# Kernel tuning notes

Hardware: AMD Instinct MI355X
Metric: run time of the kernel (lower is better)

The kernel has to match this reference:

```python
import jax, jax.numpy as jnp
import numpy as np

EPS_STD = 1e-6
EPS_LN = 1e-5


def layernorm(x, g, b):
    m = jnp.mean(x, axis=-1, keepdims=True)
    v = jnp.mean((x - m) ** 2, axis=-1, keepdims=True)
    return (x - m) * jax.lax.rsqrt(v + EPS_LN) * g + b


def res_block(x, w1, b1, g1, bb1, w2, b2, g2, bb2):
    # in_dim == out_dim for all blocks here -> skip is Identity
    h = jax.nn.relu(layernorm(x @ w1 + b1, g1, bb1))
    h = layernorm(h @ w2 + b2, g2, bb2)
    return jax.nn.relu(h + x)


def setup_inputs() -> dict:
    key = jax.random.key(0)
    ks = jax.random.split(key, 12)
    B, N, C_in, C_out, K, M = 8, 2048, 64, 128, 24, 1024
    D = 2 * C_in  # 128 == C_out
    inp = {
        'features': jax.random.normal(ks[0], (B, N, C_in), jnp.float32),
        'xyz': jax.random.normal(ks[1], (B, N, 3), jnp.float32),
        'fps_idx': jax.random.randint(ks[2], (B, M), 0, N, jnp.int32),
        'alpha': jnp.ones((1, 1, 1, C_in), jnp.float32),
        'beta': jnp.zeros((1, 1, 1, C_in), jnp.float32),
    }
    # stacked params for 2 pre blocks (D->D) and 2 pos blocks (C_out->C_out); D == C_out
    def blk(k, n, d):
        k1, k2 = jax.random.split(k)
        return dict(
            w1=jax.random.normal(k1, (n, d, d), jnp.float32) * 0.05,
            b1=jnp.zeros((n, 1, d), jnp.float32),
            g1=jnp.ones((n, 1, d), jnp.float32),
            bb1=jnp.zeros((n, 1, d), jnp.float32),
            w2=jax.random.normal(k2, (n, d, d), jnp.float32) * 0.05,
            b2=jnp.zeros((n, 1, d), jnp.float32),
            g2=jnp.ones((n, 1, d), jnp.float32),
            bb2=jnp.zeros((n, 1, d), jnp.float32),
        )
    for pfx, k in (('pre', ks[3]), ('pos', ks[4])):
        for name, v in blk(k, 2, D).items():
            inp[pfx + '_' + name] = v
    return inp


def reference(features, xyz, fps_idx, alpha, beta,
              pre_w1, pre_b1, pre_g1, pre_bb1, pre_w2, pre_b2, pre_g2, pre_bb2,
              pos_w1, pos_b1, pos_g1, pos_bb1, pos_w2, pos_b2, pos_g2, pos_bb2):
    B, N, C = features.shape
    K = 24
    # kNN on xyz via squared distances (same ordering as cdist topk smallest)
    x2 = jnp.sum(xyz * xyz, axis=-1)  # (B,N)
    d2 = x2[:, :, None] + x2[:, None, :] - 2.0 * jnp.einsum('bnd,bmd->bnm', xyz, xyz)
    _, idx = jax.lax.top_k(-d2, K)  # (B,N,K)
    gather = jax.vmap(lambda f, i: f[i])
    grouped = gather(features, idx)  # (B,N,K,C)
    # GeometricAffine: normalize over neighbor dim (torch std is unbiased, ddof=1)
    mean = jnp.mean(grouped, axis=-2, keepdims=True)
    std = jnp.maximum(jnp.std(grouped, axis=-2, keepdims=True, ddof=1), EPS_STD)
    grouped = (grouped - mean) / std * alpha + beta
    center = features[:, :, None, :]
    local = jnp.concatenate(
        [jnp.broadcast_to(center, grouped.shape), grouped - center], axis=-1)  # (B,N,K,2C)
    h = local.reshape(B * N * K, 2 * C)
    for i in range(pre_w1.shape[0]):
        h = res_block(h, pre_w1[i], pre_b1[i], pre_g1[i], pre_bb1[i],
                      pre_w2[i], pre_b2[i], pre_g2[i], pre_bb2[i])
    h = h.reshape(B, N, K, -1).max(axis=2)  # (B,N,C_out)
    h = h.reshape(B * N, -1)
    for i in range(pos_w1.shape[0]):
        h = res_block(h, pos_w1[i], pos_b1[i], pos_g1[i], pos_bb1[i],
                      pos_w2[i], pos_b2[i], pos_g2[i], pos_bb2[i])
    h = h.reshape(B, N, -1)
    new_xyz = gather(xyz, fps_idx)
    new_features = gather(h, fps_idx)
    return new_features, new_xyz
```

## Files before the change

kernel.cpp:

```cpp
#include <hip/hip_runtime.h>


typedef _Float16 half8 __attribute__((ext_vector_type(8)));
typedef _Float16 h2v   __attribute__((ext_vector_type(2)));
typedef float    f32x4 __attribute__((ext_vector_type(4)));
typedef unsigned long long u64;

#define DEVINL __device__ __forceinline__

union H8 { half8 v; h2v p[4]; int w[4]; };

DEVINL f32x4 splat4(float s) { f32x4 r = {s, s, s, s}; return r; }

DEVINL _Float16 hmax1(_Float16 a, _Float16 b) { return a > b ? a : b; }
DEVINL h2v hmax2v(h2v a, h2v b) {
  h2v r; r[0] = hmax1(a[0], b[0]); r[1] = hmax1(a[1], b[1]); return r;
}
DEVINL h2v cvt2h(float lo, float hi) {
  return __builtin_bit_cast(h2v, __builtin_amdgcn_cvt_pkrtz(lo, hi));
}
DEVINL half8 hmax8(half8 a, half8 b) {
  H8 A, B, R; A.v = a; B.v = b;
  #pragma unroll
  for (int e = 0; e < 4; ++e) R.p[e] = hmax2v(A.p[e], B.p[e]);
  return R.v;
}
DEVINL half8 shfl_h8(half8 x, int m) {
  H8 X; X.v = x;
  #pragma unroll
  for (int e = 0; e < 4; ++e) X.w[e] = __shfl_xor(X.w[e], m);
  return X.v;
}

DEVINL float dpp_add16(float x) {
  int v = __builtin_bit_cast(int, x);
  x += __builtin_bit_cast(float, __builtin_amdgcn_update_dpp(v, v, 0xB1, 0xF, 0xF, true));
  v = __builtin_bit_cast(int, x);
  x += __builtin_bit_cast(float, __builtin_amdgcn_update_dpp(v, v, 0x4E, 0xF, 0xF, true));
  v = __builtin_bit_cast(int, x);
  x += __builtin_bit_cast(float, __builtin_amdgcn_update_dpp(v, v, 0x141, 0xF, 0xF, true));
  v = __builtin_bit_cast(int, x);
  x += __builtin_bit_cast(float, __builtin_amdgcn_update_dpp(v, v, 0x140, 0xF, 0xF, true));
  return x;
}

DEVINL void stH(_Float16* L, int row, int col, _Float16 v) {
  const int b2 = col * 2;
  *(_Float16*)((char*)L + row * 256 + (((b2 >> 4) ^ (row & 7)) << 4) + (b2 & 15)) = v;
}
DEVINL half8 ldA(const _Float16* L, int row, int ch) {
  return *(const half8*)((const char*)L + row * 256 + ((ch ^ (row & 7)) << 4));
}
DEVINL void stA(_Float16* L, int row, int ch, half8 v) {
  *(half8*)((char*)L + row * 256 + ((ch ^ (row & 7)) << 4)) = v;
}

template<int MT>
DEVINL void mm_dev(const _Float16* L, const _Float16* __restrict__ W, f32x4 acc[MT][9], int lane) {
  const int g = lane >> 4, r = lane & 15;
  #pragma unroll
  for (int s = 0; s < 4; ++s) {
    half8 bfr[9];
    #pragma unroll
    for (int t = 0; t < 9; ++t)
      bfr[t] = *(const half8*)(W + (((s * 9 + t) * 64 + lane) * 8));
    #pragma unroll
    for (int mt = 0; mt < MT; ++mt) {
      const half8 a = ldA(L, mt * 16 + r, s * 4 + g);
      #pragma unroll
      for (int t = 0; t < 9; ++t)
        acc[mt][t] = __builtin_amdgcn_mfma_f32_16x16x32_f16(a, bfr[t], acc[mt][t], 0, 0, 0);
    }
  }
}

template<int MT>
DEVINL void epi_ln(f32x4 acc[MT][9], const float* __restrict__ bv, const float* __restrict__ gv,
                   const float* __restrict__ bbv, int lane) {
  const int cr = lane & 15;
  const f32x4 bp0 = *(const f32x4*)(bv + cr * 8),  bp1 = *(const f32x4*)(bv + cr * 8 + 4);
  const f32x4 gp0 = *(const f32x4*)(gv + cr * 8),  gp1 = *(const f32x4*)(gv + cr * 8 + 4);
  const f32x4 ap0 = *(const f32x4*)(bbv + cr * 8), ap1 = *(const f32x4*)(bbv + cr * 8 + 4);
  const f32x4 bs4 = bp0 + bp1;
  const float sb = dpp_add16(bs4[0] + bs4[1] + bs4[2] + bs4[3]);
  #pragma unroll
  for (int mt = 0; mt < MT; ++mt) {
    f32x4 sq4 = splat4(0.f);
    #pragma unroll
    for (int t = 0; t < 8; ++t) {
      const float bias = (t < 4) ? bp0[t & 3] : bp1[t & 3];
      acc[mt][t] = acc[mt][t] + splat4(bias);
      sq4 = sq4 + acc[mt][t] * acc[mt][t];
    }
    #pragma unroll
    for (int q = 0; q < 4; ++q) sq4[q] = dpp_add16(sq4[q]);
    const f32x4 mean = (acc[mt][8] + splat4(sb)) * splat4(1.f / 128.f);
    f32x4 rstd;
    #pragma unroll
    for (int q = 0; q < 4; ++q) {
      const float var = fmaxf(sq4[q] * (1.f / 128.f) - mean[q] * mean[q], 0.f);
      rstd[q] = rsqrtf(var + 1e-5f);
    }
    #pragma unroll
    for (int t = 0; t < 8; ++t) {
      const float gs = (t < 4) ? gp0[t & 3] : gp1[t & 3];
      const float as = (t < 4) ? ap0[t & 3] : ap1[t & 3];
      acc[mt][t] = (acc[mt][t] - mean) * rstd * splat4(gs) + splat4(as);
    }
  }
}

template<int MT, int MODE>
DEVINL void res_block_dev(_Float16* L, const _Float16* __restrict__ W1, const _Float16* __restrict__ W2,
                          const float* b1, const float* g1, const float* bb1,
                          const float* b2, const float* g2, const float* bb2,
                          half8 xres[MT][4], int lane, float* __restrict__ gdst) {
  const int g = lane >> 4, cr = lane & 15;
  const h2v zero2 = {(_Float16)0, (_Float16)0};
  f32x4 acc[MT][9];
  #pragma unroll
  for (int mt = 0; mt < MT; ++mt)
    #pragma unroll
    for (int t = 0; t < 9; ++t) acc[mt][t] = splat4(0.f);
  mm_dev<MT>(L, W1, acc, lane);
  epi_ln<MT>(acc, b1, g1, bb1, lane);
  __threadfence_block();
  #pragma unroll
  for (int mt = 0; mt < MT; ++mt)
    #pragma unroll
    for (int q = 0; q < 4; ++q) {
      H8 hv;
      #pragma unroll
      for (int e = 0; e < 4; ++e)
        hv.p[e] = hmax2v(cvt2h(acc[mt][2 * e][q], acc[mt][2 * e + 1][q]), zero2);
      stA(L, mt * 16 + 4 * g + q, cr, hv.v);
    }
  #pragma unroll
  for (int mt = 0; mt < MT; ++mt)
    #pragma unroll
    for (int t = 0; t < 9; ++t) acc[mt][t] = splat4(0.f);
  __threadfence_block();
  mm_dev<MT>(L, W2, acc, lane);
  epi_ln<MT>(acc, b2, g2, bb2, lane);
  if constexpr (MODE == 0) __threadfence_block();
  #pragma unroll
  for (int mt = 0; mt < MT; ++mt)
    #pragma unroll
    for (int q = 0; q < 4; ++q) {
      const int row = mt * 16 + 4 * g + q;
      if constexpr (MODE == 2) {
        f32x4 lo, hi;
        #pragma unroll
        for (int e = 0; e < 4; ++e) {
          lo[e] = fmaxf(acc[mt][e][q]     + (float)xres[mt][q][e],     0.f);
          hi[e] = fmaxf(acc[mt][e + 4][q] + (float)xres[mt][q][e + 4], 0.f);
        }
        *(f32x4*)(gdst + row * 128 + cr * 8)     = lo;
        *(f32x4*)(gdst + row * 128 + cr * 8 + 4) = hi;
      } else {
        H8 s;
        #pragma unroll
        for (int e = 0; e < 4; ++e)
          s.p[e] = cvt2h(acc[mt][2 * e][q], acc[mt][2 * e + 1][q]);
        H8 z; z.v = s.v + xres[mt][q];
        #pragma unroll
        for (int e = 0; e < 4; ++e) z.p[e] = hmax2v(z.p[e], zero2);
        xres[mt][q] = z.v;
        if constexpr (MODE == 0) stA(L, row, cr, z.v);
      }
    }
  if constexpr (MODE == 0) __threadfence_block();
}

__global__ __launch_bounds__(256) void k_pack(const float* __restrict__ preW1, const float* __restrict__ preW2,
                                              const float* __restrict__ posW1, const float* __restrict__ posW2,
                                              _Float16* __restrict__ wp) {
  const int o = blockIdx.x * 256 + threadIdx.x;
  const int mat = o / 18432, rem = o % 18432;
  const int frag = rem >> 9, li = (rem >> 3) & 63, j = rem & 7;
  const int s = frag / 9, t = frag % 9;
  const int k = s * 32 + ((li >> 4) << 3) + j;
  const int blk = (mat >> 1) & 1, which = mat & 1;
  const float* base = (mat < 4) ? (which ? preW2 : preW1) : (which ? posW2 : posW1);
  const float* Wm = base + blk * 16384;
  float val;
  if (t < 8) {
    val = Wm[k * 128 + (li & 15) * 8 + t];
  } else {
    float ssum = 0.f;
    for (int n = 0; n < 128; ++n) ssum += Wm[k * 128 + n];
    val = ssum;
  }
  wp[o] = (_Float16)val;
}

DEVINL u64 kmin(u64 a, u64 b) { return a < b ? a : b; }
DEVINL u64 kmax(u64 a, u64 b) { return a > b ? a : b; }
DEVINL u64 min8(const u64* k) {
  u64 a = kmin(k[0], k[1]), b = kmin(k[2], k[3]);
  u64 c = kmin(k[4], k[5]), d = kmin(k[6], k[7]);
  return kmin(kmin(a, b), kmin(c, d));
}
DEVINL void inv8(u64* k, int j) {
  #pragma unroll
  for (int s = 0; s < 8; ++s) k[s] = (s == j) ? ~0ULL : k[s];
}
DEVINL u64 bitonic64(u64 v, int lane) {
  #pragma unroll
  for (int k = 2; k <= 64; k <<= 1) {
    #pragma unroll
    for (int j = k >> 1; j > 0; j >>= 1) {
      const u64 o = __shfl_xor(v, j);
      const bool up = ((lane & k) == 0);
      const bool lower = ((lane & j) == 0);
      v = (lower == up) ? kmin(v, o) : kmax(v, o);
    }
  }
  return v;
}

__global__ __launch_bounds__(256) void k_knn(const float* __restrict__ xyz, int* __restrict__ idxout) {
  __shared__ float sx[2048], sy[2048], sz[2048];
  __shared__ u64 scand[4][64];
  const int b = blockIdx.x >> 9;
  const int qbase = (blockIdx.x & 511) * 4;
  const float* xb = xyz + (size_t)b * 2048 * 3;
  for (int i = threadIdx.x; i < 2048; i += 256) {
    sx[i] = xb[i * 3 + 0]; sy[i] = xb[i * 3 + 1]; sz[i] = xb[i * 3 + 2];
  }
  __syncthreads();
  const int wid = threadIdx.x >> 6, lane = threadIdx.x & 63;
  const int q = qbase + wid;
  const float qx = sx[q], qy = sy[q], qz = sz[q];
  const float q2 = qx * qx + qy * qy + qz * qz;
  u64 key[32];
  u64 lmin = ~0ULL;
  #pragma unroll
  for (int j = 0; j < 32; ++j) {
    const int m = j * 64 + lane;
    const float mx = sx[m], my = sy[m], mz = sz[m];
    const float m2 = mx * mx + my * my + mz * mz;
    const float d = fmaxf(q2 + m2 - 2.f * (qx * mx + qy * my + qz * mz), 0.f);
    key[j] = ((u64)__builtin_bit_cast(unsigned, d) << 32) | (unsigned)m;
    lmin = kmin(lmin, key[j]);
  }
  const u64 t = __shfl(bitonic64(lmin, lane), 23);
  int c = 0;
  #pragma unroll
  for (int j = 0; j < 32; ++j) c += (key[j] <= t) ? 1 : 0;
  int inc = c;
  #pragma unroll
  for (int off = 1; off < 64; off <<= 1) {
    const int n = __shfl_up(inc, off);
    if (lane >= off) inc += n;
  }
  const int T = __shfl(inc, 63);
  if (T <= 64) {
    int idx = inc - c;
    #pragma unroll
    for (int j = 0; j < 32; ++j)
      if (key[j] <= t) { scand[wid][idx] = key[j]; ++idx; }
    __threadfence_block();
    u64 cand = (lane < T) ? scand[wid][lane] : ~0ULL;
    cand = bitonic64(cand, lane);
    if (lane < 24) idxout[(size_t)(b * 2048 + q) * 24 + lane] = (int)(unsigned)cand;
  } else {
    u64 gk[4];
    #pragma unroll
    for (int g4 = 0; g4 < 4; ++g4) gk[g4] = min8(key + g4 * 8);
    int keep = 0;
    #pragma unroll 1
    for (int r = 0; r < 24; ++r) {
      u64 kk = kmin(kmin(gk[0], gk[1]), kmin(gk[2], gk[3]));
      #pragma unroll
      for (int off = 32; off >= 1; off >>= 1) kk = kmin(__shfl_xor(kk, off), kk);
      const unsigned wm = (unsigned)kk;
      if (lane == r) keep = (int)wm;
      if (lane == (int)(wm & 63)) {
        const int j = (int)(wm >> 6);
        if (j < 16) {
          if (j < 8) { inv8(key,      j);      gk[0] = min8(key);      }
          else       { inv8(key + 8,  j - 8);  gk[1] = min8(key + 8);  }
        } else {
          if (j < 24){ inv8(key + 16, j - 16); gk[2] = min8(key + 16); }
          else       { inv8(key + 24, j - 24); gk[3] = min8(key + 24); }
        }
      }
    }
    if (lane < 24) idxout[(size_t)(b * 2048 + q) * 24 + lane] = keep;
  }
}

__global__ __launch_bounds__(256, 1) void k_pre(
    const float* __restrict__ features, const int* __restrict__ idxin,
    const _Float16* __restrict__ wp, const float* __restrict__ alpha, const float* __restrict__ beta,
    const float* __restrict__ b1, const float* __restrict__ g1, const float* __restrict__ bb1,
    const float* __restrict__ b2, const float* __restrict__ g2, const float* __restrict__ bb2,
    _Float16* __restrict__ h0) {
  __shared__ _Float16 lds[4][48 * 128];
  const int wid = threadIdx.x >> 6, lane = threadIdx.x & 63;
  _Float16* L = lds[wid];
  const int wgl = blockIdx.x * 4 + wid;
  const int p0 = wgl * 2;
  const int b = p0 >> 11;
  const float* fb = features + (size_t)b * 2048 * 64;
  {
    const int c = lane;
    const float al = alpha[c], be = beta[c];
    #pragma unroll 1
    for (int pp = 0; pp < 2; ++pp) {
      const int p = p0 + pp;
      const int n = p & 2047;
      const int* ip = idxin + (size_t)p * 24;
      const float center = fb[n * 64 + c];
      float v[24]; float su = 0.f, sq = 0.f;
      #pragma unroll
      for (int k = 0; k < 24; ++k) {
        v[k] = fb[ip[k] * 64 + c];
        su += v[k]; sq = fmaf(v[k], v[k], sq);
      }
      const float mean = su * (1.f / 24.f);
      const float var = fmaxf((sq - 24.f * mean * mean) * (1.f / 23.f), 0.f);
      const float rs = 1.f / fmaxf(sqrtf(var), 1e-6f);
      const float c1 = rs * al;
      const float c0 = be - mean * c1 - center;
      const _Float16 ch = (_Float16)center;
      #pragma unroll
      for (int k = 0; k < 24; ++k) {
        const int row = pp * 24 + k;
        stH(L, row, c, ch);
        stH(L, row, 64 + c, (_Float16)fmaf(v[k], c1, c0));
      }
    }
  }
  __threadfence_block();
  const int g = lane >> 4, cr = lane & 15;
  half8 xres[3][4];
  #pragma unroll
  for (int mt = 0; mt < 3; ++mt)
    #pragma unroll
    for (int q = 0; q < 4; ++q)
      xres[mt][q] = ldA(L, mt * 16 + 4 * g + q, cr);
  res_block_dev<3, 0>(L, wp,         wp + 18432,  b1,       g1,       bb1,       b2,       g2,       bb2,       xres, lane, nullptr);
  res_block_dev<3, 1>(L, wp + 36864, wp + 55296,  b1 + 128, g1 + 128, bb1 + 128, b2 + 128, g2 + 128, bb2 + 128, xres, lane, nullptr);
  half8 m0 = hmax8(hmax8(xres[0][0], xres[0][1]), hmax8(xres[0][2], xres[0][3]));
  m0 = hmax8(m0, shfl_h8(m0, 16));
  m0 = hmax8(m0, shfl_h8(m0, 32));
  half8 m1 = hmax8(hmax8(xres[1][0], xres[1][1]), hmax8(xres[1][2], xres[1][3]));
  m1 = hmax8(m1, shfl_h8(m1, 16));
  const half8 m1o = shfl_h8(m1, 32);
  half8 m2 = hmax8(hmax8(xres[2][0], xres[2][1]), hmax8(xres[2][2], xres[2][3]));
  m2 = hmax8(m2, shfl_h8(m2, 16));
  m2 = hmax8(m2, shfl_h8(m2, 32));
  if (g == 0) *(half8*)(h0 + (size_t)p0 * 128 + cr * 8)       = hmax8(m0, m1);
  if (g == 1) *(half8*)(h0 + (size_t)(p0 + 1) * 128 + cr * 8) = hmax8(m2, m1o);
}

__global__ __launch_bounds__(128, 2) void k_pos(
    const _Float16* __restrict__ h0, const _Float16* __restrict__ wp,
    const float* __restrict__ b1, const float* __restrict__ g1, const float* __restrict__ bb1,
    const float* __restrict__ b2, const float* __restrict__ g2, const float* __restrict__ bb2,
    float* __restrict__ h1) {
  __shared__ _Float16 lds[2][32 * 128];
  const int wid = threadIdx.x >> 6, lane = threadIdx.x & 63;
  _Float16* L = lds[wid];
  const int wgl = blockIdx.x * 2 + wid;
  const size_t rowbase = (size_t)wgl * 32;
  #pragma unroll
  for (int i = 0; i < 8; ++i) {
    const int r = i * 4 + (lane >> 4), ch = lane & 15;
    const half8 tv = *(const half8*)(h0 + (rowbase + r) * 128 + ch * 8);
    stA(L, r, ch, tv);
  }
  __threadfence_block();
  const int g = lane >> 4, cr = lane & 15;
  half8 xres[2][4];
  #pragma unroll
  for (int mt = 0; mt < 2; ++mt)
    #pragma unroll
    for (int q = 0; q < 4; ++q)
      xres[mt][q] = ldA(L, mt * 16 + 4 * g + q, cr);
  res_block_dev<2, 0>(L, wp + 73728,  wp + 92160,  b1,       g1,       bb1,       b2,       g2,       bb2,       xres, lane, nullptr);
  res_block_dev<2, 2>(L, wp + 110592, wp + 129024, b1 + 128, g1 + 128, bb1 + 128, b2 + 128, g2 + 128, bb2 + 128, xres, lane, h1 + rowbase * 128);
}

__global__ __launch_bounds__(256) void k_gather(const float* __restrict__ h1, const float* __restrict__ xyz,
                                                const int* __restrict__ fps, float* __restrict__ out) {
  const int i = blockIdx.x * 256 + threadIdx.x;
  const int FEAT4 = 8 * 1024 * 32;
  if (i < FEAT4) {
    const int c4 = i & 31, m = (i >> 5) & 1023, b = i >> 15;
    const int n = fps[b * 1024 + m];
    const f32x4 v = *(const f32x4*)(h1 + ((size_t)(b * 2048 + n)) * 128 + c4 * 4);
    *(f32x4*)(out + (size_t)i * 4) = v;
  } else {
    const int jj = i - FEAT4;
    if (jj < 8 * 1024 * 3) {
      const int dd = jj % 3, m = (jj / 3) & 1023, b = jj / 3072;
      const int n = fps[b * 1024 + m];
      out[8 * 1024 * 128 + jj] = xyz[((size_t)(b * 2048 + n)) * 3 + dd];
    }
  }
}

extern "C" void kernel_launch(void* const* d_in, const int* in_sizes, int n_in,
                              void* d_out, int out_size, void* d_ws, size_t ws_size,
                              hipStream_t stream) {
  const float* features = (const float*)d_in[0];
  const float* xyz      = (const float*)d_in[1];
  const int*   fps      = (const int*)d_in[2];
  const float* alpha    = (const float*)d_in[3];
  const float* beta     = (const float*)d_in[4];
  const float* pre_w1   = (const float*)d_in[5];
  const float* pre_b1   = (const float*)d_in[6];
  const float* pre_g1   = (const float*)d_in[7];
  const float* pre_bb1  = (const float*)d_in[8];
  const float* pre_w2   = (const float*)d_in[9];
  const float* pre_b2   = (const float*)d_in[10];
  const float* pre_g2   = (const float*)d_in[11];
  const float* pre_bb2  = (const float*)d_in[12];
  const float* pos_w1   = (const float*)d_in[13];
  const float* pos_b1   = (const float*)d_in[14];
  const float* pos_g1   = (const float*)d_in[15];
  const float* pos_bb1  = (const float*)d_in[16];
  const float* pos_w2   = (const float*)d_in[17];
  const float* pos_b2   = (const float*)d_in[18];
  const float* pos_g2   = (const float*)d_in[19];
  const float* pos_bb2  = (const float*)d_in[20];
  (void)in_sizes; (void)n_in; (void)out_size; (void)ws_size;

  char* ws = (char*)d_ws;
  _Float16* wp   = (_Float16*)(ws);
  int*      idxb = (int*)(ws + 524288);
  _Float16* h0   = (_Float16*)(ws + 2097152);
  float*    h1   = (float*)(ws + 6291456);

  k_pack<<<dim3(576), dim3(256), 0, stream>>>(pre_w1, pre_w2, pos_w1, pos_w2, wp);
  k_knn<<<dim3(4096), dim3(256), 0, stream>>>(xyz, idxb);
  k_pre<<<dim3(2048), dim3(256), 0, stream>>>(features, idxb, wp, alpha, beta,
      pre_b1, pre_g1, pre_bb1, pre_b2, pre_g2, pre_bb2, h0);
  k_pos<<<dim3(256), dim3(128), 0, stream>>>(h0, wp,
      pos_b1, pos_g1, pos_bb1, pos_b2, pos_g2, pos_bb2, h1);
  k_gather<<<dim3(1120), dim3(256), 0, stream>>>(h1, xyz, fps, (float*)d_out);
}
```

Baseline: 191.3 us.

## Stage pre-block weights in shared LDS and process one point per wave

k_pre now gives each wave a single point (24 neighbor rows padded to a 32-row tile) instead of two points in 48 rows, and launches twice as many blocks. The four waves of a block cooperatively copy each 128x128 fp16 weight matrix into shared LDS behind __syncthreads, so B fragments are read from LDS instead of global or L2. The aim is to cut global weight traffic and raise occupancy. In exchange, a quarter of the MFMA rows are padding, each block adds four staging passes and barriers, and padded rows must be masked before the max reduction.

```diff
diff --git a/kernel.cpp b/kernel.cpp
--- a/kernel.cpp
+++ b/kernel.cpp
@@ -55,6 +55,14 @@
   *(half8*)((char*)L + row * 256 + ((ch ^ (row & 7)) << 4)) = v;
 }
 
+DEVINL void stageW(_Float16* Wl, const _Float16* __restrict__ Wsrc, int tid) {
+  #pragma unroll
+  for (int i = 0; i < 9; ++i) {
+    const int o = (tid + i * 256) * 8;
+    *(half8*)(Wl + o) = *(const half8*)(Wsrc + o);
+  }
+}
+
 template<int MT>
 DEVINL void mm_dev(const _Float16* L, const _Float16* __restrict__ W, f32x4 acc[MT][9], int lane) {
   const int g = lane >> 4, r = lane & 15;
@@ -64,6 +72,25 @@
     #pragma unroll
     for (int t = 0; t < 9; ++t)
       bfr[t] = *(const half8*)(W + (((s * 9 + t) * 64 + lane) * 8));
+    #pragma unroll
+    for (int mt = 0; mt < MT; ++mt) {
+      const half8 a = ldA(L, mt * 16 + r, s * 4 + g);
+      #pragma unroll
+      for (int t = 0; t < 9; ++t)
+        acc[mt][t] = __builtin_amdgcn_mfma_f32_16x16x32_f16(a, bfr[t], acc[mt][t], 0, 0, 0);
+    }
+  }
+}
+
+template<int MT>
+DEVINL void mm_lds(const _Float16* L, const _Float16* Wl, f32x4 acc[MT][9], int lane) {
+  const int g = lane >> 4, r = lane & 15;
+  #pragma unroll
+  for (int s = 0; s < 4; ++s) {
+    half8 bfr[9];
+    #pragma unroll
+    for (int t = 0; t < 9; ++t)
+      bfr[t] = *(const half8*)(Wl + ((s * 9 + t) * 64 + lane) * 8);
     #pragma unroll
     for (int mt = 0; mt < MT; ++mt) {
       const half8 a = ldA(L, mt * 16 + r, s * 4 + g);
@@ -108,6 +135,63 @@
       acc[mt][t] = (acc[mt][t] - mean) * rstd * splat4(gs) + splat4(as);
     }
   }
+}
+
+template<int MODE>
+DEVINL void res_block_pre(_Float16* L, _Float16* Wl,
+                          const _Float16* __restrict__ W1, const _Float16* __restrict__ W2,
+                          const float* b1, const float* g1, const float* bb1,
+                          const float* b2, const float* g2, const float* bb2,
+                          half8 xres[2][4], int lane, int tid) {
+  const int g = lane >> 4, cr = lane & 15;
+  const h2v zero2 = {(_Float16)0, (_Float16)0};
+  f32x4 acc[2][9];
+  __syncthreads();
+  stageW(Wl, W1, tid);
+  __syncthreads();
+  #pragma unroll
+  for (int mt = 0; mt < 2; ++mt)
+    #pragma unroll
+    for (int t = 0; t < 9; ++t) acc[mt][t] = splat4(0.f);
+  mm_lds<2>(L, Wl, acc, lane);
+  epi_ln<2>(acc, b1, g1, bb1, lane);
+  __threadfence_block();
+  #pragma unroll
+  for (int mt = 0; mt < 2; ++mt)
+    #pragma unroll
+    for (int q = 0; q < 4; ++q) {
+      H8 hv;
+      #pragma unroll
+      for (int e = 0; e < 4; ++e)
+        hv.p[e] = hmax2v(cvt2h(acc[mt][2 * e][q], acc[mt][2 * e + 1][q]), zero2);
+      stA(L, mt * 16 + 4 * g + q, cr, hv.v);
+    }
+  __threadfence_block();
+  __syncthreads();
+  stageW(Wl, W2, tid);
+  __syncthreads();
+  #pragma unroll
+  for (int mt = 0; mt < 2; ++mt)
+    #pragma unroll
+    for (int t = 0; t < 9; ++t) acc[mt][t] = splat4(0.f);
+  mm_lds<2>(L, Wl, acc, lane);
+  epi_ln<2>(acc, b2, g2, bb2, lane);
+  if constexpr (MODE == 0) __threadfence_block();
+  #pragma unroll
+  for (int mt = 0; mt < 2; ++mt)
+    #pragma unroll
+    for (int q = 0; q < 4; ++q) {
+      H8 s;
+      #pragma unroll
+      for (int e = 0; e < 4; ++e)
+        s.p[e] = cvt2h(acc[mt][2 * e][q], acc[mt][2 * e + 1][q]);
+      H8 z; z.v = s.v + xres[mt][q];
+      #pragma unroll
+      for (int e = 0; e < 4; ++e) z.p[e] = hmax2v(z.p[e], zero2);
+      xres[mt][q] = z.v;
+      if constexpr (MODE == 0) stA(L, mt * 16 + 4 * g + q, cr, z.v);
+    }
+  if constexpr (MODE == 0) __threadfence_block();
 }
 
 template<int MT, int MODE>
@@ -297,63 +381,64 @@
     const float* __restrict__ b1, const float* __restrict__ g1, const float* __restrict__ bb1,
     const float* __restrict__ b2, const float* __restrict__ g2, const float* __restrict__ bb2,
     _Float16* __restrict__ h0) {
-  __shared__ _Float16 lds[4][48 * 128];
-  const int wid = threadIdx.x >> 6, lane = threadIdx.x & 63;
-  _Float16* L = lds[wid];
-  const int wgl = blockIdx.x * 4 + wid;
-  const int p0 = wgl * 2;
-  const int b = p0 >> 11;
+  __shared__ _Float16 Alds[4][32 * 128];
+  __shared__ _Float16 Wlds[18432];
+  const int tid = threadIdx.x;
+  const int wid = tid >> 6, lane = tid & 63;
+  _Float16* L = Alds[wid];
+  const int p = blockIdx.x * 4 + wid;
+  const int b = p >> 11;
+  const int n = p & 2047;
   const float* fb = features + (size_t)b * 2048 * 64;
   {
     const int c = lane;
     const float al = alpha[c], be = beta[c];
-    #pragma unroll 1
-    for (int pp = 0; pp < 2; ++pp) {
-      const int p = p0 + pp;
-      const int n = p & 2047;
-      const int* ip = idxin + (size_t)p * 24;
-      const float center = fb[n * 64 + c];
-      float v[24]; float su = 0.f, sq = 0.f;
-      #pragma unroll
-      for (int k = 0; k < 24; ++k) {
-        v[k] = fb[ip[k] * 64 + c];
-        su += v[k]; sq = fmaf(v[k], v[k], sq);
-      }
-      const float mean = su * (1.f / 24.f);
-      const float var = fmaxf((sq - 24.f * mean * mean) * (1.f / 23.f), 0.f);
-      const float rs = 1.f / fmaxf(sqrtf(var), 1e-6f);
-      const float c1 = rs * al;
-      const float c0 = be - mean * c1 - center;
-      const _Float16 ch = (_Float16)center;
-      #pragma unroll
-      for (int k = 0; k < 24; ++k) {
-        const int row = pp * 24 + k;
-        stH(L, row, c, ch);
-        stH(L, row, 64 + c, (_Float16)fmaf(v[k], c1, c0));
-      }
+    const int* ip = idxin + (size_t)p * 24;
+    const float center = fb[n * 64 + c];
+    float v[24]; float su = 0.f, sq = 0.f;
+    #pragma unroll
+    for (int k = 0; k < 24; ++k) {
+      v[k] = fb[ip[k] * 64 + c];
+      su += v[k]; sq = fmaf(v[k], v[k], sq);
+    }
+    const float mean = su * (1.f / 24.f);
+    const float var = fmaxf((sq - 24.f * mean * mean) * (1.f / 23.f), 0.f);
+    const float rs = 1.f / fmaxf(sqrtf(var), 1e-6f);
+    const float c1 = rs * al;
+    const float c0 = be - mean * c1 - center;
+    const _Float16 ch = (_Float16)center;
+    #pragma unroll
+    for (int k = 0; k < 24; ++k) {
+      stH(L, k, c, ch);
+      stH(L, k, 64 + c, (_Float16)fmaf(v[k], c1, c0));
     }
   }
   __threadfence_block();
   const int g = lane >> 4, cr = lane & 15;
-  half8 xres[3][4];
-  #pragma unroll
-  for (int mt = 0; mt < 3; ++mt)
+  half8 xres[2][4];
+  #pragma unroll
+  for (int mt = 0; mt < 2; ++mt)
     #pragma unroll
     for (int q = 0; q < 4; ++q)
       xres[mt][q] = ldA(L, mt * 16 + 4 * g + q, cr);
-  res_block_dev<3, 0>(L, wp,         wp + 18432,  b1,       g1,       bb1,       b2,       g2,       bb2,       xres, lane, nullptr);
-  res_block_dev<3, 1>(L, wp + 36864, wp + 55296,  b1 + 128, g1 + 128, bb1 + 128, b2 + 128, g2 + 128, bb2 + 128, xres, lane, nullptr);
+  res_block_pre<0>(L, Wlds, wp,         wp + 18432,
+                   b1,       g1,       bb1,       b2,       g2,       bb2,       xres, lane, tid);
+  res_block_pre<1>(L, Wlds, wp + 36864, wp + 55296,
+                   b1 + 128, g1 + 128, bb1 + 128, b2 + 128, g2 + 128, bb2 + 128, xres, lane, tid);
   half8 m0 = hmax8(hmax8(xres[0][0], xres[0][1]), hmax8(xres[0][2], xres[0][3]));
   m0 = hmax8(m0, shfl_h8(m0, 16));
   m0 = hmax8(m0, shfl_h8(m0, 32));
   half8 m1 = hmax8(hmax8(xres[1][0], xres[1][1]), hmax8(xres[1][2], xres[1][3]));
+  if (g >= 2) {
+    H8 z;
+    #pragma unroll
+    for (int e = 0; e < 4; ++e) z.w[e] = 0;
+    m1 = z.v;
+  }
   m1 = hmax8(m1, shfl_h8(m1, 16));
-  const half8 m1o = shfl_h8(m1, 32);
-  half8 m2 = hmax8(hmax8(xres[2][0], xres[2][1]), hmax8(xres[2][2], xres[2][3]));
-  m2 = hmax8(m2, shfl_h8(m2, 16));
-  m2 = hmax8(m2, shfl_h8(m2, 32));
-  if (g == 0) *(half8*)(h0 + (size_t)p0 * 128 + cr * 8)       = hmax8(m0, m1);
-  if (g == 1) *(half8*)(h0 + (size_t)(p0 + 1) * 128 + cr * 8) = hmax8(m2, m1o);
+  m1 = hmax8(m1, shfl_h8(m1, 32));
+  const half8 mm = hmax8(m0, m1);
+  if (g == 0) *(half8*)(h0 + (size_t)p * 128 + cr * 8) = mm;
 }
 
 __global__ __launch_bounds__(128, 2) void k_pos(
@@ -437,7 +522,7 @@
 
   k_pack<<<dim3(576), dim3(256), 0, stream>>>(pre_w1, pre_w2, pos_w1, pos_w2, wp);
   k_knn<<<dim3(4096), dim3(256), 0, stream>>>(xyz, idxb);
-  k_pre<<<dim3(2048), dim3(256), 0, stream>>>(features, idxb, wp, alpha, beta,
+  k_pre<<<dim3(4096), dim3(256), 0, stream>>>(features, idxb, wp, alpha, beta,
       pre_b1, pre_g1, pre_bb1, pre_b2, pre_g2, pre_bb2, h0);
   k_pos<<<dim3(256), dim3(128), 0, stream>>>(h0, wp,
       pos_b1, pos_g1, pos_bb1, pos_b2, pos_g2, pos_bb2, h1);
```

After: 251.9 us. 1.32x slower.

## Split pre-MLP into two kernel variants with one-point-per-wave padded tiles

Applied to the files above, without the earlier changes.

The pre-stage kernel is split in two. k_preA keeps the old two-points-per-wave, 48-row scheme but now covers only the first half of the points. k_preB handles the second half with one point per wave in 32-row tiles, padding 24 rows up to 32. It uses ping-pong LDS buffers and a new gemm_ln_B routine that computes the LayerNorm mean directly rather than from a packed weight-sum column. The LN epilogue is also folded into a single FMA per element, and launch bounds allow two blocks per CU, trading some wasted padded MFMA work for different occupancy and register pressure.

```diff
diff --git a/kernel.cpp b/kernel.cpp
--- a/kernel.cpp
+++ b/kernel.cpp
@@ -105,7 +105,9 @@
     for (int t = 0; t < 8; ++t) {
       const float gs = (t < 4) ? gp0[t & 3] : gp1[t & 3];
       const float as = (t < 4) ? ap0[t & 3] : ap1[t & 3];
-      acc[mt][t] = (acc[mt][t] - mean) * rstd * splat4(gs) + splat4(as);
+      const f32x4 c1 = rstd * splat4(gs);
+      const f32x4 c0 = splat4(as) - mean * c1;
+      acc[mt][t] = acc[mt][t] * c1 + c0;
     }
   }
 }
@@ -172,6 +174,80 @@
   if constexpr (MODE == 0) __threadfence_block();
 }
 
+template<bool RES>
+DEVINL void gemm_ln_B(const _Float16* src, _Float16* dst, const _Float16* rsrc,
+                      const _Float16* __restrict__ W,
+                      const float* __restrict__ bv, const float* __restrict__ gv,
+                      const float* __restrict__ bbv, int lane) {
+  const int g = lane >> 4, r = lane & 15, cr = r;
+  const h2v zero2 = {(_Float16)0, (_Float16)0};
+  f32x4 acc[2][8];
+  #pragma unroll
+  for (int mt = 0; mt < 2; ++mt)
+    #pragma unroll
+    for (int t = 0; t < 8; ++t) acc[mt][t] = splat4(0.f);
+  #pragma unroll
+  for (int s = 0; s < 4; ++s) {
+    const half8 a0 = ldA(src, r,      s * 4 + g);
+    const half8 a1 = ldA(src, 16 + r, s * 4 + g);
+    #pragma unroll
+    for (int hb = 0; hb < 2; ++hb) {
+      half8 bfr[4];
+      #pragma unroll
+      for (int t = 0; t < 4; ++t)
+        bfr[t] = *(const half8*)(W + (((s * 9 + hb * 4 + t) * 64 + lane) * 8));
+      #pragma unroll
+      for (int t = 0; t < 4; ++t) {
+        acc[0][hb * 4 + t] = __builtin_amdgcn_mfma_f32_16x16x32_f16(a0, bfr[t], acc[0][hb * 4 + t], 0, 0, 0);
+        acc[1][hb * 4 + t] = __builtin_amdgcn_mfma_f32_16x16x32_f16(a1, bfr[t], acc[1][hb * 4 + t], 0, 0, 0);
+      }
+    }
+  }
+  const f32x4 bp0 = *(const f32x4*)(bv + cr * 8),  bp1 = *(const f32x4*)(bv + cr * 8 + 4);
+  const f32x4 gp0 = *(const f32x4*)(gv + cr * 8),  gp1 = *(const f32x4*)(gv + cr * 8 + 4);
+  const f32x4 ap0 = *(const f32x4*)(bbv + cr * 8), ap1 = *(const f32x4*)(bbv + cr * 8 + 4);
+  #pragma unroll
+  for (int mt = 0; mt < 2; ++mt) {
+    f32x4 su4 = splat4(0.f), sq4 = splat4(0.f);
+    #pragma unroll
+    for (int t = 0; t < 8; ++t) {
+      const float bias = (t < 4) ? bp0[t & 3] : bp1[t & 3];
+      const f32x4 x = acc[mt][t] + splat4(bias);
+      acc[mt][t] = x;
+      su4 = su4 + x;
+      sq4 = sq4 + x * x;
+    }
+    #pragma unroll
+    for (int q = 0; q < 4; ++q) { su4[q] = dpp_add16(su4[q]); sq4[q] = dpp_add16(sq4[q]); }
+    #pragma unroll
+    for (int q = 0; q < 4; ++q) {
+      const int row = mt * 16 + 4 * g + q;
+      const float mean = su4[q] * (1.f / 128.f);
+      const float var  = fmaxf(sq4[q] * (1.f / 128.f) - mean * mean, 0.f);
+      const float rstd = rsqrtf(var + 1e-5f);
+      float y[8];
+      #pragma unroll
+      for (int t = 0; t < 8; ++t) {
+        const float gs = (t < 4) ? gp0[t & 3] : gp1[t & 3];
+        const float as = (t < 4) ? ap0[t & 3] : ap1[t & 3];
+        const float c1 = rstd * gs;
+        const float c0 = as - mean * c1;
+        y[t] = fmaf(acc[mt][t][q], c1, c0);
+      }
+      if constexpr (RES) {
+        const half8 xv = ldA(rsrc, row, cr);
+        #pragma unroll
+        for (int t = 0; t < 8; ++t) y[t] += (float)xv[t];
+      }
+      H8 o;
+      #pragma unroll
+      for (int e = 0; e < 4; ++e)
+        o.p[e] = hmax2v(cvt2h(y[2 * e], y[2 * e + 1]), zero2);
+      stA(dst, row, cr, o.v);
+    }
+  }
+}
+
 __global__ __launch_bounds__(256) void k_pack(const float* __restrict__ preW1, const float* __restrict__ preW2,
                                               const float* __restrict__ posW1, const float* __restrict__ posW2,
                                               _Float16* __restrict__ wp) {
@@ -291,17 +367,17 @@
   }
 }
 
-__global__ __launch_bounds__(256, 1) void k_pre(
+__global__ __launch_bounds__(256, 2) void k_preA(
     const float* __restrict__ features, const int* __restrict__ idxin,
     const _Float16* __restrict__ wp, const float* __restrict__ alpha, const float* __restrict__ beta,
     const float* __restrict__ b1, const float* __restrict__ g1, const float* __restrict__ bb1,
     const float* __restrict__ b2, const float* __restrict__ g2, const float* __restrict__ bb2,
-    _Float16* __restrict__ h0) {
+    _Float16* __restrict__ h0, int pbase0) {
   __shared__ _Float16 lds[4][48 * 128];
   const int wid = threadIdx.x >> 6, lane = threadIdx.x & 63;
   _Float16* L = lds[wid];
   const int wgl = blockIdx.x * 4 + wid;
-  const int p0 = wgl * 2;
+  const int p0 = pbase0 + wgl * 2;
   const int b = p0 >> 11;
   const float* fb = features + (size_t)b * 2048 * 64;
   {
@@ -341,8 +417,10 @@
     #pragma unroll
     for (int q = 0; q < 4; ++q)
       xres[mt][q] = ldA(L, mt * 16 + 4 * g + q, cr);
-  res_block_dev<3, 0>(L, wp,         wp + 18432,  b1,       g1,       bb1,       b2,       g2,       bb2,       xres, lane, nullptr);
-  res_block_dev<3, 1>(L, wp + 36864, wp + 55296,  b1 + 128, g1 + 128, bb1 + 128, b2 + 128, g2 + 128, bb2 + 128, xres, lane, nullptr);
+  res_block_dev<3, 0>(L, wp,         wp + 18432,
+                      b1,       g1,       bb1,       b2,       g2,       bb2,       xres, lane, nullptr);
+  res_block_dev<3, 1>(L, wp + 36864, wp + 55296,
+                      b1 + 128, g1 + 128, bb1 + 128, b2 + 128, g2 + 128, bb2 + 128, xres, lane, nullptr);
   half8 m0 = hmax8(hmax8(xres[0][0], xres[0][1]), hmax8(xres[0][2], xres[0][3]));
   m0 = hmax8(m0, shfl_h8(m0, 16));
   m0 = hmax8(m0, shfl_h8(m0, 32));
@@ -354,6 +432,66 @@
   m2 = hmax8(m2, shfl_h8(m2, 32));
   if (g == 0) *(half8*)(h0 + (size_t)p0 * 128 + cr * 8)       = hmax8(m0, m1);
   if (g == 1) *(half8*)(h0 + (size_t)(p0 + 1) * 128 + cr * 8) = hmax8(m2, m1o);
+}
+
+__global__ __launch_bounds__(256, 2) void k_preB(
+    const float* __restrict__ features, const int* __restrict__ idxin,
+    const _Float16* __restrict__ wp, const float* __restrict__ alpha, const float* __restrict__ beta,
+    const float* __restrict__ b1, const float* __restrict__ g1, const float* __restrict__ bb1,
+    const float* __restrict__ b2, const float* __restrict__ g2, const float* __restrict__ bb2,
+    _Float16* __restrict__ h0, int pbase0) {
+  __shared__ _Float16 AB[4][2][32 * 128];
+  const int tid = threadIdx.x, wid = tid >> 6, lane = tid & 63;
+  _Float16* Xr = AB[wid][0];
+  _Float16* Hr = AB[wid][1];
+  const int p = pbase0 + blockIdx.x * 4 + wid;
+  const int b = p >> 11, n = p & 2047;
+  const float* fb = features + (size_t)b * 2048 * 64;
+  {
+    const int c = lane;
+    const float al = alpha[c], be = beta[c];
+    const int* ip = idxin + (size_t)p * 24;
+    const float center = fb[n * 64 + c];
+    float v[24]; float su = 0.f, sq = 0.f;
+    #pragma unroll
+    for (int k = 0; k < 24; ++k) {
+      v[k] = fb[ip[k] * 64 + c];
+      su += v[k]; sq = fmaf(v[k], v[k], sq);
+    }
+    const float mean = su * (1.f / 24.f);
+    const float var = fmaxf((sq - 24.f * mean * mean) * (1.f / 23.f), 0.f);
+    const float rs = 1.f / fmaxf(sqrtf(var), 1e-6f);
+    const float c1 = rs * al;
+    const float c0 = be - mean * c1 - center;
+    const _Float16 ch = (_Float16)center;
+    #pragma unroll
+    for (int k = 0; k < 24; ++k) {
+      stH(Xr, k, c, ch);
+      stH(Xr, k, 64 + c, (_Float16)fmaf(v[k], c1, c0));
+    }
+    const _Float16 z0 = (_Float16)0;
+    #pragma unroll
+    for (int k = 24; k < 32; ++k) {
+      stH(Xr, k, c, z0);
+      stH(Xr, k, 64 + c, z0);
+    }
+  }
+  __threadfence_block();
+  gemm_ln_B<false>(Xr, Hr, nullptr, wp,         b1,       g1,       bb1,       lane);
+  __threadfence_block();
+  gemm_ln_B<true >(Hr, Xr, Xr,      wp + 18432, b2,       g2,       bb2,       lane);
+  __threadfence_block();
+  gemm_ln_B<false>(Xr, Hr, nullptr, wp + 36864, b1 + 128, g1 + 128, bb1 + 128, lane);
+  __threadfence_block();
+  gemm_ln_B<true >(Hr, Xr, Xr,      wp + 55296, b2 + 128, g2 + 128, bb2 + 128, lane);
+  __threadfence_block();
+  const int gq = lane >> 4, cr = lane & 15;
+  half8 m = ldA(Xr, gq * 6, cr);
+  #pragma unroll
+  for (int k = 1; k < 6; ++k) m = hmax8(m, ldA(Xr, gq * 6 + k, cr));
+  m = hmax8(m, shfl_h8(m, 16));
+  m = hmax8(m, shfl_h8(m, 32));
+  if (gq == 0) *(half8*)(h0 + (size_t)p * 128 + cr * 8) = m;
 }
 
 __global__ __launch_bounds__(128, 2) void k_pos(
@@ -437,8 +575,10 @@
 
   k_pack<<<dim3(576), dim3(256), 0, stream>>>(pre_w1, pre_w2, pos_w1, pos_w2, wp);
   k_knn<<<dim3(4096), dim3(256), 0, stream>>>(xyz, idxb);
-  k_pre<<<dim3(2048), dim3(256), 0, stream>>>(features, idxb, wp, alpha, beta,
-      pre_b1, pre_g1, pre_bb1, pre_b2, pre_g2, pre_bb2, h0);
+  k_preA<<<dim3(1024), dim3(256), 0, stream>>>(features, idxb, wp, alpha, beta,
+      pre_b1, pre_g1, pre_bb1, pre_b2, pre_g2, pre_bb2, h0, 0);
+  k_preB<<<dim3(2048), dim3(256), 0, stream>>>(features, idxb, wp, alpha, beta,
+      pre_b1, pre_g1, pre_bb1, pre_b2, pre_g2, pre_bb2, h0, 8192);
   k_pos<<<dim3(256), dim3(128), 0, stream>>>(h0, wp,
       pos_b1, pos_g1, pos_bb1, pos_b2, pos_g2, pos_bb2, h1);
   k_gather<<<dim3(1120), dim3(256), 0, stream>>>(h1, xyz, fps, (float*)d_out);
```

Measured after the change: 194.6 us. About the same (+1.7%).
